# Kernel tuning notes

Hardware: AMD Instinct MI355X
Metric: run time of the kernel (lower is better)

## Reference

```python
import jax, jax.numpy as jnp
import numpy as np

SIGMA_LIKELIHOOD = 0.1  # hardcoded in the original forward
LOG_SQRT_2PI = 0.5 * float(np.log(2.0 * np.pi))


def _expected_mu(pred):
    """Vectorized calculateExpectedValues over the batch.
    pred: [B, 7] in molecule order O2, N2, H2, CO2, H2O, CH4, NH3.
    Returns mu: [B, 7] expected abundance per molecule (0 for unclassified).
    """
    O2, N2, H2, CO2, H2O, CH4, NH3 = (pred[:, i] for i in range(7))
    H = 2 * H2 + 2 * H2O + 3 * NH3 + 4 * CH4
    C = CO2 + CH4
    O = 2 * O2 + 2 * CO2 + H2O
    N = 2 * N2 + NH3

    condA = H > 2 * O + 4 * C
    mA1 = condA & (3 * N < H - 2 * O - 4 * C)
    mA2 = condA & ~mA1
    mB = ~condA & (2 * O > H + 4 * C)
    mC = ~condA & ~mB & (jnp.abs(H + C + O + N - 1.0) < 1e-3)

    def sd(num, den, m):  # masked safe divide (avoids NaN in unselected branches)
        return jnp.where(m, num / jnp.where(m, den, 1.0), 0.0)

    z = jnp.zeros_like(H)
    # branch A1: D = H - N - 2C
    dA1 = H - N - 2 * C
    muA1 = jnp.stack([z, z, sd(H - 2 * O - 4 * C - 3 * N, dA1, mA1), z,
                      sd(2 * O, dA1, mA1), sd(2 * C, dA1, mA1), sd(2 * N, dA1, mA1)], axis=-1)
    # branch A2: D = H + 2C + 3N + 4O
    dA2 = H + 2 * C + 3 * N + 4 * O
    muA2 = jnp.stack([z, sd(3 * N + 4 * C + 2 * O - H, dA2, mA2), z, z,
                      sd(6 * O, dA2, mA2), sd(6 * C, dA2, mA2), sd(2 * H - 8 * C - 4 * O, dA2, mA2)], axis=-1)
    # branch B: D = H + 2O + 2N
    dB = H + 2 * O + 2 * N
    muB = jnp.stack([sd(2 * O - H - 4 * C, dB, mB), sd(2 * N, dB, mB), z,
                     sd(4 * C, dB, mB), sd(2 * H, dB, mB), z, z], axis=-1)
    # branch C: D1 = H + 2O + 2N, D2 = 2H + 4O + 4N
    d1 = H + 2 * O + 2 * N
    d2 = 2 * H + 4 * O + 4 * N
    muC = jnp.stack([z, sd(2 * N, d1, mC), z, sd(2 * O + 4 * C - H, d2, mC),
                     sd(H + 2 * O - 4 * C, d1, mC), sd(H - 2 * O + 4 * C, d2, mC), z], axis=-1)
    # masks are mutually exclusive -> sum selects the right branch (unknown -> 0)
    return muA1 + muA2 + muB + muC


def setup_inputs() -> dict:
    key = jax.random.key(0)
    k1, k2, k3, k4 = jax.random.split(key, 4)
    B, S = 8192, 4096
    predAbun = jax.random.uniform(k1, (B, 7), dtype=jnp.float32)
    sigmaPrior = jax.random.uniform(k2, (B, 7), dtype=jnp.float32) * 0.5 + 0.1
    yReal = jax.random.normal(k3, (B, S), dtype=jnp.float32)
    ySim = jax.random.normal(k4, (B, S), dtype=jnp.float32)
    return {"predAbun": predAbun, "sigmaPrior": sigmaPrior, "yReal": yReal, "ySim": ySim}


def reference(predAbun, sigmaPrior, yReal, ySim):
    # prior: batched vectorization of the per-sample Python loop in calculatePrior
    mu = _expected_mu(predAbun)                                  # [B, 7]
    per_elem = (LOG_SQRT_2PI + jnp.log(sigmaPrior)
                + (predAbun - mu) ** 2 / (2.0 * sigmaPrior ** 2))  # [B, 7]
    prior = jnp.sum(per_elem) / predAbun.shape[0]                # scalar (mean over batch of per-sample sums)
    # likelihood: per-sample gaussian NLL of spectra
    mse = jnp.mean((yReal - ySim) ** 2, axis=1)                  # [B]
    likelihood = mse / (2.0 * SIGMA_LIKELIHOOD ** 2)             # [B]
    posterior = likelihood + prior                               # [B]
    return posterior
```

## Files before the change

### kernel.cpp

```cpp
#include <hip/hip_runtime.h>
#include <math.h>

#define LOG_SQRT_2PI 0.9189385332046727f

__global__ void zero_ws(float* ws) {
    if (threadIdx.x == 0 && blockIdx.x == 0) ws[0] = 0.0f;
}

__global__ __launch_bounds__(256) void prior_kernel(
        const float* __restrict__ pred,
        const float* __restrict__ sigma,
        float* __restrict__ ws, int B) {
    int b = blockIdx.x * blockDim.x + threadIdx.x;
    float s = 0.0f;
    if (b < B) {
        const float* p  = pred  + (size_t)b * 7;
        const float* sg = sigma + (size_t)b * 7;
        float O2 = p[0], N2 = p[1], H2 = p[2], CO2 = p[3];
        float H2O = p[4], CH4 = p[5], NH3 = p[6];

        float H = 2.f*H2 + 2.f*H2O + 3.f*NH3 + 4.f*CH4;
        float C = CO2 + CH4;
        float O = 2.f*O2 + 2.f*CO2 + H2O;
        float N = 2.f*N2 + NH3;

        float mu0=0.f, mu1=0.f, mu2=0.f, mu3=0.f, mu4=0.f, mu5=0.f, mu6=0.f;

        bool condA = (H > 2.f*O + 4.f*C);
        if (condA) {
            if (3.f*N < H - 2.f*O - 4.f*C) {
                float D = H - N - 2.f*C;
                mu2 = (H - 2.f*O - 4.f*C - 3.f*N) / D;
                mu4 = (2.f*O) / D;
                mu5 = (2.f*C) / D;
                mu6 = (2.f*N) / D;
            } else {
                float D = H + 2.f*C + 3.f*N + 4.f*O;
                mu1 = (3.f*N + 4.f*C + 2.f*O - H) / D;
                mu4 = (6.f*O) / D;
                mu5 = (6.f*C) / D;
                mu6 = (2.f*H - 8.f*C - 4.f*O) / D;
            }
        } else if (2.f*O > H + 4.f*C) {
            float D = H + 2.f*O + 2.f*N;
            mu0 = (2.f*O - H - 4.f*C) / D;
            mu1 = (2.f*N) / D;
            mu3 = (4.f*C) / D;
            mu4 = (2.f*H) / D;
        } else if (fabsf(H + C + O + N - 1.0f) < 1e-3f) {
            float D1 = H + 2.f*O + 2.f*N;
            float D2 = 2.f*H + 4.f*O + 4.f*N;
            mu1 = (2.f*N) / D1;
            mu3 = (2.f*O + 4.f*C - H) / D2;
            mu4 = (H + 2.f*O - 4.f*C) / D1;
            mu5 = (H - 2.f*O + 4.f*C) / D2;
        }

        float mu[7] = {mu0, mu1, mu2, mu3, mu4, mu5, mu6};
        #pragma unroll
        for (int i = 0; i < 7; ++i) {
            float d = p[i] - mu[i];
            float sgi = sg[i];
            s += LOG_SQRT_2PI + logf(sgi) + d * d / (2.0f * sgi * sgi);
        }
    }

    #pragma unroll
    for (int off = 32; off > 0; off >>= 1) s += __shfl_down(s, off, 64);
    __shared__ float wsum[4];
    int lane = threadIdx.x & 63, w = threadIdx.x >> 6;
    if (lane == 0) wsum[w] = s;
    __syncthreads();
    if (threadIdx.x == 0) {
        atomicAdd(ws, wsum[0] + wsum[1] + wsum[2] + wsum[3]);
    }
}

__global__ __launch_bounds__(256) void loss_kernel(
        const float* __restrict__ yReal,
        const float* __restrict__ ySim,
        const float* __restrict__ ws,
        float* __restrict__ out, int S, float inv_b) {
    int b = blockIdx.x;
    const float4* yr = (const float4*)(yReal + (size_t)b * S);
    const float4* ys = (const float4*)(ySim  + (size_t)b * S);
    int n4 = S >> 2;

    float s = 0.0f;
    for (int i = threadIdx.x; i < n4; i += blockDim.x) {
        float4 a = yr[i];
        float4 c = ys[i];
        float d0 = a.x - c.x, d1 = a.y - c.y;
        float d2 = a.z - c.z, d3 = a.w - c.w;
        s += d0*d0 + d1*d1 + d2*d2 + d3*d3;
    }

    #pragma unroll
    for (int off = 32; off > 0; off >>= 1) s += __shfl_down(s, off, 64);
    __shared__ float wsum[4];
    int lane = threadIdx.x & 63, w = threadIdx.x >> 6;
    if (lane == 0) wsum[w] = s;
    __syncthreads();
    if (threadIdx.x == 0) {
        float mse = (wsum[0] + wsum[1] + wsum[2] + wsum[3]) / (float)S;
        out[b] = mse * 50.0f + ws[0] * inv_b;
    }
}

extern "C" void kernel_launch(void* const* d_in, const int* in_sizes, int n_in,
                              void* d_out, int out_size, void* d_ws, size_t ws_size,
                              hipStream_t stream) {
    const float* pred  = (const float*)d_in[0];
    const float* sigma = (const float*)d_in[1];
    const float* yReal = (const float*)d_in[2];
    const float* ySim  = (const float*)d_in[3];
    float* out = (float*)d_out;
    float* ws  = (float*)d_ws;

    int B = in_sizes[0] / 7;
    int S = in_sizes[2] / B;

    zero_ws<<<1, 64, 0, stream>>>(ws);
    int pb = (B + 255) / 256;
    prior_kernel<<<pb, 256, 0, stream>>>(pred, sigma, ws, B);
    loss_kernel<<<B, 256, 0, stream>>>(yReal, ySim, ws, out, S, 1.0f / (float)B);
}
```

Measured before the change: 51.72 us.

## Replace atomic prior reduction with per-block partials summed inside loss kernel

Drops the zero-init kernel and the global atomicAdd. The prior kernel now writes one partial sum per block, and each loss block folds those partials into its own block reduction. The loss kernel is also templated with a fully unrolled fixed trip count for the common S values, with a generic fallback that handles a scalar tail. This removes one launch and the atomic, at the cost of every loss block redundantly reading up to 256 partials.

```diff
diff --git a/kernel.cpp b/kernel.cpp
--- a/kernel.cpp
+++ b/kernel.cpp
@@ -3,17 +3,12 @@
 
 #define LOG_SQRT_2PI 0.9189385332046727f
 
-__global__ void zero_ws(float* ws) {
-    if (threadIdx.x == 0 && blockIdx.x == 0) ws[0] = 0.0f;
-}
-
-__global__ __launch_bounds__(256) void prior_kernel(
+__global__ __launch_bounds__(256) void prior_partials(
         const float* __restrict__ pred,
         const float* __restrict__ sigma,
-        float* __restrict__ ws, int B) {
-    int b = blockIdx.x * blockDim.x + threadIdx.x;
+        float* __restrict__ ws, int B, int pb) {
     float s = 0.0f;
-    if (b < B) {
+    for (int b = blockIdx.x * 256 + threadIdx.x; b < B; b += pb * 256) {
         const float* p  = pred  + (size_t)b * 7;
         const float* sg = sigma + (size_t)b * 7;
         float O2 = p[0], N2 = p[1], H2 = p[2], CO2 = p[3];
@@ -71,40 +66,77 @@
     int lane = threadIdx.x & 63, w = threadIdx.x >> 6;
     if (lane == 0) wsum[w] = s;
     __syncthreads();
-    if (threadIdx.x == 0) {
-        atomicAdd(ws, wsum[0] + wsum[1] + wsum[2] + wsum[3]);
-    }
+    if (threadIdx.x == 0) ws[blockIdx.x] = wsum[0] + wsum[1] + wsum[2] + wsum[3];
 }
 
-__global__ __launch_bounds__(256) void loss_kernel(
+template <int NITER>
+__global__ __launch_bounds__(256) void loss_kernel_t(
         const float* __restrict__ yReal,
         const float* __restrict__ ySim,
-        const float* __restrict__ ws,
-        float* __restrict__ out, int S, float inv_b) {
+        const float* __restrict__ partials,
+        float* __restrict__ out, int S, float c_mse, float c_prior, int pb) {
     int b = blockIdx.x;
     const float4* yr = (const float4*)(yReal + (size_t)b * S);
     const float4* ys = (const float4*)(ySim  + (size_t)b * S);
-    int n4 = S >> 2;
+
+    float u = (threadIdx.x < pb) ? partials[threadIdx.x] * c_prior : 0.0f;
 
     float s = 0.0f;
-    for (int i = threadIdx.x; i < n4; i += blockDim.x) {
+    #pragma unroll
+    for (int k = 0; k < NITER; ++k) {
+        int i = threadIdx.x + k * 256;
         float4 a = yr[i];
         float4 c = ys[i];
         float d0 = a.x - c.x, d1 = a.y - c.y;
         float d2 = a.z - c.z, d3 = a.w - c.w;
         s += d0*d0 + d1*d1 + d2*d2 + d3*d3;
     }
+    u += s * c_mse;
 
     #pragma unroll
-    for (int off = 32; off > 0; off >>= 1) s += __shfl_down(s, off, 64);
+    for (int off = 32; off > 0; off >>= 1) u += __shfl_down(u, off, 64);
     __shared__ float wsum[4];
     int lane = threadIdx.x & 63, w = threadIdx.x >> 6;
-    if (lane == 0) wsum[w] = s;
+    if (lane == 0) wsum[w] = u;
     __syncthreads();
-    if (threadIdx.x == 0) {
-        float mse = (wsum[0] + wsum[1] + wsum[2] + wsum[3]) / (float)S;
-        out[b] = mse * 50.0f + ws[0] * inv_b;
+    if (threadIdx.x == 0) out[b] = wsum[0] + wsum[1] + wsum[2] + wsum[3];
+}
+
+__global__ __launch_bounds__(256) void loss_kernel_g(
+        const float* __restrict__ yReal,
+        const float* __restrict__ ySim,
+        const float* __restrict__ partials,
+        float* __restrict__ out, int S, float c_mse, float c_prior, int pb) {
+    int b = blockIdx.x;
+    const float* yr = yReal + (size_t)b * S;
+    const float* ys = ySim  + (size_t)b * S;
+
+    float u = (threadIdx.x < pb) ? partials[threadIdx.x] * c_prior : 0.0f;
+
+    float s = 0.0f;
+    int n4 = S >> 2;
+    const float4* yr4 = (const float4*)yr;
+    const float4* ys4 = (const float4*)ys;
+    for (int i = threadIdx.x; i < n4; i += 256) {
+        float4 a = yr4[i];
+        float4 c = ys4[i];
+        float d0 = a.x - c.x, d1 = a.y - c.y;
+        float d2 = a.z - c.z, d3 = a.w - c.w;
+        s += d0*d0 + d1*d1 + d2*d2 + d3*d3;
     }
+    for (int i = (n4 << 2) + threadIdx.x; i < S; i += 256) {
+        float d = yr[i] - ys[i];
+        s += d * d;
+    }
+    u += s * c_mse;
+
+    #pragma unroll
+    for (int off = 32; off > 0; off >>= 1) u += __shfl_down(u, off, 64);
+    __shared__ float wsum[4];
+    int lane = threadIdx.x & 63, w = threadIdx.x >> 6;
+    if (lane == 0) wsum[w] = u;
+    __syncthreads();
+    if (threadIdx.x == 0) out[b] = wsum[0] + wsum[1] + wsum[2] + wsum[3];
 }
 
 extern "C" void kernel_launch(void* const* d_in, const int* in_sizes, int n_in,
@@ -120,8 +152,19 @@
     int B = in_sizes[0] / 7;
     int S = in_sizes[2] / B;
 
-    zero_ws<<<1, 64, 0, stream>>>(ws);
     int pb = (B + 255) / 256;
-    prior_kernel<<<pb, 256, 0, stream>>>(pred, sigma, ws, B);
-    loss_kernel<<<B, 256, 0, stream>>>(yReal, ySim, ws, out, S, 1.0f / (float)B);
+    if (pb > 256) pb = 256;
+
+    prior_partials<<<pb, 256, 0, stream>>>(pred, sigma, ws, B, pb);
+
+    float c_mse   = 50.0f / (float)S;
+    float c_prior = 1.0f / (float)B;
+
+    if ((S & 3) == 0 && (S >> 2) == 1024) {
+        loss_kernel_t<4><<<B, 256, 0, stream>>>(yReal, ySim, ws, out, S, c_mse, c_prior, pb);
+    } else if ((S & 3) == 0 && (S >> 2) == 2048) {
+        loss_kernel_t<8><<<B, 256, 0, stream>>>(yReal, ySim, ws, out, S, c_mse, c_prior, pb);
+    } else {
+        loss_kernel_g<<<B, 256, 0, stream>>>(yReal, ySim, ws, out, S, c_mse, c_prior, pb);
+    }
 }
```

Result: faster. 47.32 us (-8.5%).
